# Kernel optimization log

Measured on AMD Instinct MI355X. Metric: run time of the kernel, lower is better.

## Reference

```python
import jax, jax.numpy as jnp
import numpy as np

START_TAG = 2
STOP_TAG = 3
NEG = -10000.0


def _lstm_dir(x, w_ih, w_hh, b_ih, b_hh, h0, c0):
    """Single-direction LSTM over x:[T,F]. PyTorch gate order i,f,g,o."""
    xp = x @ w_ih.T + b_ih  # [T, 4H] - big GEMM done once

    def step(carry, xt):
        h, c = carry
        g = xt + h @ w_hh.T + b_hh
        i, f, gg, o = jnp.split(g, 4)
        c = jax.nn.sigmoid(f) * c + jax.nn.sigmoid(i) * jnp.tanh(gg)
        h = jax.nn.sigmoid(o) * jnp.tanh(c)
        return (h, c), h

    _, hs = jax.lax.scan(step, (h0, c0), xp)
    return hs  # [T, H]


def _viterbi(feats, transitions):
    # feats: [T, n_tags]; transitions[next, prev]
    n = transitions.shape[0]
    init = jnp.full((n,), NEG, feats.dtype).at[START_TAG].set(0.0)

    def step(fv, feat):
        scores = fv[None, :] + transitions          # [next, prev]
        bptr = jnp.argmax(scores, axis=1)           # best prev per next
        return jnp.max(scores, axis=1) + feat, bptr

    fv, bptrs = jax.lax.scan(step, init, feats)
    terminal = fv + transitions[STOP_TAG]
    best = jnp.argmax(terminal)
    score = terminal[best]

    def back(tag, bp):
        return bp[tag], tag  # emit tag at step t, carry tag at t-1

    _, path = jax.lax.scan(back, best, bptrs, reverse=True)
    return score, path  # scalar, [T] int32


def setup_inputs() -> dict:
    key = jax.random.key(0)
    T, F, H = 4096, 1024, 2048
    H2 = H // 2
    NTAG = 4
    ks = jax.random.split(key, 16)
    s_ih = 1.0 / np.sqrt(H2)

    def u(k, shape, s):
        return jax.random.uniform(k, shape, jnp.float32, -s, s)

    transitions = jax.random.normal(ks[13], (NTAG, NTAG), jnp.float32)
    transitions = transitions.at[START_TAG, :].set(NEG)
    transitions = transitions.at[:, STOP_TAG].set(NEG)

    return {
        "sentence": jax.random.normal(ks[0], (T, F), jnp.float32),
        "h0": jax.random.normal(ks[1], (2, 1, H2), jnp.float32),
        "c0": jax.random.normal(ks[2], (2, 1, H2), jnp.float32),
        "w_ih_f": u(ks[3], (4 * H2, F), s_ih),
        "w_hh_f": u(ks[4], (4 * H2, H2), s_ih),
        "b_ih_f": u(ks[5], (4 * H2,), s_ih),
        "b_hh_f": u(ks[6], (4 * H2,), s_ih),
        "w_ih_b": u(ks[7], (4 * H2, F), s_ih),
        "w_hh_b": u(ks[8], (4 * H2, H2), s_ih),
        "b_ih_b": u(ks[9], (4 * H2,), s_ih),
        "b_hh_b": u(ks[10], (4 * H2,), s_ih),
        "w_tag": u(ks[11], (NTAG, H), 1.0 / np.sqrt(H)),
        "b_tag": u(ks[12], (NTAG,), 1.0 / np.sqrt(H)),
        "transitions": transitions,
    }


def reference(sentence, h0, c0, w_ih_f, w_hh_f, b_ih_f, b_hh_f,
              w_ih_b, w_hh_b, b_ih_b, b_hh_b, w_tag, b_tag, transitions):
    # Bidirectional LSTM, batch=1 (torch stacks directions on dim 0 of h0/c0)
    h_fwd = _lstm_dir(sentence, w_ih_f, w_hh_f, b_ih_f, b_hh_f, h0[0, 0], c0[0, 0])
    h_bwd = _lstm_dir(sentence[::-1], w_ih_b, w_hh_b, b_ih_b, b_hh_b, h0[1, 0], c0[1, 0])[::-1]
    lstm_out = jnp.concatenate([h_fwd, h_bwd], axis=-1)  # [T, hidden_dim]
    feats = lstm_out @ w_tag.T + b_tag                    # [T, 4]
    score, path = _viterbi(feats, transitions)
    return score, path
```

## Files before the change

### kernel.cpp

```cpp
#include <hip/hip_runtime.h>
#include <cstddef>
#include <cstdint>

#define T_LEN 4096
#define FDIM  1024
#define H2DIM 1024
#define GDIM  4096

#define NEGV (-10000.0f)
#define START_TAG 2
#define STOP_TAG 3

#define XP_OFF      ((size_t)0)
#define XP_BYTES    ((size_t)2 * T_LEN * GDIM * 4)
#define HIST_OFF    (XP_OFF + XP_BYTES)
#define HIST_BYTES  ((size_t)T_LEN * 2048 * 4)
#define FEATS_OFF   (HIST_OFF + HIST_BYTES)
#define FEATS_BYTES ((size_t)T_LEN * 4 * 4)
#define SLOTS_OFF   (FEATS_OFF + FEATS_BYTES)
#define SLOTS_BYTES ((size_t)2 * 2 * 1024 * 8)
#define WS_NEED     (SLOTS_OFF + SLOTS_BYTES)

__device__ __forceinline__ float sigm(float x) { return 1.0f / (1.0f + expf(-x)); }

__global__ __launch_bounds__(256)
void xp_gemm(const float* __restrict__ x,
             const float* __restrict__ w_f, const float* __restrict__ w_b,
             const float* __restrict__ bi_f, const float* __restrict__ bh_f,
             const float* __restrict__ bi_b, const float* __restrict__ bh_b,
             float* __restrict__ xp)
{
    const int tid = threadIdx.x;
    const int dir = blockIdx.z;
    const int j0  = blockIdx.x * 128;
    const int t0  = blockIdx.y * 128;
    const float* __restrict__ w  = dir ? w_b  : w_f;
    const float* __restrict__ bi = dir ? bi_b : bi_f;
    const float* __restrict__ bh = dir ? bh_b : bh_f;

    __shared__ float As[32][133];
    __shared__ float Bs[32][133];

    const int tm0 = (tid & 15) * 8;
    const int tn0 = (tid >> 4) * 8;

    float acc[8][8];
    #pragma unroll
    for (int i = 0; i < 8; ++i)
        #pragma unroll
        for (int j = 0; j < 8; ++j) acc[i][j] = 0.f;

    const int lrow = tid >> 3;
    const int lkq  = (tid & 7) * 4;

    for (int kb = 0; kb < FDIM; kb += 32) {
        #pragma unroll
        for (int hh = 0; hh < 4; ++hh) {
            const int r  = lrow + hh * 32;
            const int tg = t0 + r;
            const int sr = dir ? (T_LEN - 1 - tg) : tg;
            const float4 av = *(const float4*)&x[(size_t)sr * FDIM + kb + lkq];
            As[lkq+0][r] = av.x; As[lkq+1][r] = av.y; As[lkq+2][r] = av.z; As[lkq+3][r] = av.w;
            const float4 bv = *(const float4*)&w[(size_t)(j0 + r) * FDIM + kb + lkq];
            Bs[lkq+0][r] = bv.x; Bs[lkq+1][r] = bv.y; Bs[lkq+2][r] = bv.z; Bs[lkq+3][r] = bv.w;
        }
        __syncthreads();
        #pragma unroll
        for (int k = 0; k < 32; ++k) {
            const float4 a0 = *(const float4*)&As[k][tm0];
            const float4 a1 = *(const float4*)&As[k][tm0 + 4];
            const float4 b0 = *(const float4*)&Bs[k][tn0];
            const float4 b1 = *(const float4*)&Bs[k][tn0 + 4];
            const float av[8] = {a0.x,a0.y,a0.z,a0.w,a1.x,a1.y,a1.z,a1.w};
            const float bv[8] = {b0.x,b0.y,b0.z,b0.w,b1.x,b1.y,b1.z,b1.w};
            #pragma unroll
            for (int i = 0; i < 8; ++i)
                #pragma unroll
                for (int j = 0; j < 8; ++j) acc[i][j] += av[i] * bv[j];
        }
        __syncthreads();
    }

    float bias[8];
    #pragma unroll
    for (int j = 0; j < 8; ++j) { const int col = j0 + tn0 + j; bias[j] = bi[col] + bh[col]; }

    float* __restrict__ xpd = xp + (size_t)dir * T_LEN * GDIM;
    #pragma unroll
    for (int i = 0; i < 8; ++i) {
        const int tr = t0 + tm0 + i;
        float4 o0, o1;
        o0.x = acc[i][0] + bias[0]; o0.y = acc[i][1] + bias[1];
        o0.z = acc[i][2] + bias[2]; o0.w = acc[i][3] + bias[3];
        o1.x = acc[i][4] + bias[4]; o1.y = acc[i][5] + bias[5];
        o1.z = acc[i][6] + bias[6]; o1.w = acc[i][7] + bias[7];
        *(float4*)&xpd[(size_t)tr * GDIM + j0 + tn0]     = o0;
        *(float4*)&xpd[(size_t)tr * GDIM + j0 + tn0 + 4] = o1;
    }
}

__global__ __launch_bounds__(256, 1)
void lstm_scan(const float* __restrict__ xp,
               const float* __restrict__ h0,
               const float* __restrict__ c0,
               const float* __restrict__ whh_f,
               const float* __restrict__ whh_b,
               float* __restrict__ hist,
               unsigned long long* __restrict__ slots)
{
    __shared__ float wsl[32][1024];
    __shared__ float hbuf[1024];
    __shared__ float gsh[32];

    const int tid = threadIdx.x;
    const int b   = blockIdx.x;
    const int dir = b >> 7;
    const int bi  = b & 127;
    const int u0  = bi * 8;
    const int rg  = tid >> 5;
    const int kc  = tid & 31;
    const int lrb = rg * 4;

    const float* __restrict__ whh = dir ? whh_b : whh_f;
    const size_t xpbase = (size_t)dir * T_LEN * GDIM;

    for (int lr = 0; lr < 32; ++lr) {
        const int grow = ((lr >> 3) << 10) + u0 + (lr & 7);
        *(float4*)&wsl[lr][tid * 4] = *(const float4*)&whh[(size_t)grow * H2DIM + tid * 4];
    }
    *(float4*)&hbuf[tid * 4] = *(const float4*)&h0[dir * H2DIM + tid * 4];
    float creg = 0.f;
    if (tid < 8) creg = c0[dir * H2DIM + u0 + tid];

    int grows[4];
    #pragma unroll
    for (int j = 0; j < 4; ++j) {
        const int lr = lrb + j;
        grows[j] = ((lr >> 3) << 10) + u0 + (lr & 7);
    }
    float xpc[4] = {0.f, 0.f, 0.f, 0.f};
    if (kc == 0) {
        #pragma unroll
        for (int j = 0; j < 4; ++j) xpc[j] = xp[xpbase + grows[j]];
    }
    __syncthreads();

    int budget = 4000000;

    for (int t = 0; t < T_LEN; ++t) {
        float xpn[4] = {0.f, 0.f, 0.f, 0.f};
        const int tnx = (t + 1 < T_LEN) ? (t + 1) : t;
        if (kc == 0) {
            #pragma unroll
            for (int j = 0; j < 4; ++j) xpn[j] = xp[xpbase + (size_t)tnx * GDIM + grows[j]];
        }

        float p0 = 0.f, p1 = 0.f, p2 = 0.f, p3 = 0.f;
        #pragma unroll
        for (int s = 0; s < 8; ++s) {
            const int ko = s * 128 + kc * 4;
            const float4 hv = *(const float4*)&hbuf[ko];
            const float4 w0 = *(const float4*)&wsl[lrb + 0][ko];
            const float4 w1 = *(const float4*)&wsl[lrb + 1][ko];
            const float4 w2 = *(const float4*)&wsl[lrb + 2][ko];
            const float4 w3 = *(const float4*)&wsl[lrb + 3][ko];
            p0 += w0.x*hv.x + w0.y*hv.y + w0.z*hv.z + w0.w*hv.w;
            p1 += w1.x*hv.x + w1.y*hv.y + w1.z*hv.z + w1.w*hv.w;
            p2 += w2.x*hv.x + w2.y*hv.y + w2.z*hv.z + w2.w*hv.w;
            p3 += w3.x*hv.x + w3.y*hv.y + w3.z*hv.z + w3.w*hv.w;
        }
        #pragma unroll
        for (int m = 16; m >= 1; m >>= 1) {
            p0 += __shfl_xor(p0, m);
            p1 += __shfl_xor(p1, m);
            p2 += __shfl_xor(p2, m);
            p3 += __shfl_xor(p3, m);
        }
        if (kc == 0) {
            gsh[lrb + 0] = p0 + xpc[0];
            gsh[lrb + 1] = p1 + xpc[1];
            gsh[lrb + 2] = p2 + xpc[2];
            gsh[lrb + 3] = p3 + xpc[3];
        }
        __syncthreads();

        if (tid < 8) {
            const float gi = gsh[tid];
            const float gf = gsh[8 + tid];
            const float gg = gsh[16 + tid];
            const float go = gsh[24 + tid];
            const float c  = sigm(gf) * creg + sigm(gi) * tanhf(gg);
            const float h  = sigm(go) * tanhf(c);
            creg = c;
            const int tg = dir ? (T_LEN - 1 - t) : t;
            hist[(size_t)tg * 2048 + dir * H2DIM + u0 + tid] = h;
            const unsigned long long pack =
                ((unsigned long long)(unsigned)(t + 1) << 32) |
                (unsigned long long)__float_as_uint(h);
            __hip_atomic_store(&slots[((size_t)((t + 1) & 1) * 2 + dir) * H2DIM + u0 + tid],
                               pack, __ATOMIC_RELAXED, __HIP_MEMORY_SCOPE_AGENT);
        }

        if (t + 1 < T_LEN) {
            const unsigned want = (unsigned)(t + 1);
            unsigned long long* sb = &slots[((size_t)((t + 1) & 1) * 2 + dir) * H2DIM + tid * 4];
            unsigned long long v0 = 0, v1 = 0, v2 = 0, v3 = 0;
            bool g0 = false, g1 = false, g2 = false, g3 = false;
            for (;;) {
                if (!g0) v0 = __hip_atomic_load(&sb[0], __ATOMIC_RELAXED, __HIP_MEMORY_SCOPE_AGENT);
                if (!g1) v1 = __hip_atomic_load(&sb[1], __ATOMIC_RELAXED, __HIP_MEMORY_SCOPE_AGENT);
                if (!g2) v2 = __hip_atomic_load(&sb[2], __ATOMIC_RELAXED, __HIP_MEMORY_SCOPE_AGENT);
                if (!g3) v3 = __hip_atomic_load(&sb[3], __ATOMIC_RELAXED, __HIP_MEMORY_SCOPE_AGENT);
                g0 = g0 || ((unsigned)(v0 >> 32) == want);
                g1 = g1 || ((unsigned)(v1 >> 32) == want);
                g2 = g2 || ((unsigned)(v2 >> 32) == want);
                g3 = g3 || ((unsigned)(v3 >> 32) == want);
                if (g0 && g1 && g2 && g3) break;
                if (--budget <= 0) break;
                __builtin_amdgcn_s_sleep(1);
            }
            float4 hv;
            hv.x = __uint_as_float((unsigned)v0);
            hv.y = __uint_as_float((unsigned)v1);
            hv.z = __uint_as_float((unsigned)v2);
            hv.w = __uint_as_float((unsigned)v3);
            *(float4*)&hbuf[tid * 4] = hv;
        }
        __syncthreads();
        if (kc == 0) { xpc[0] = xpn[0]; xpc[1] = xpn[1]; xpc[2] = xpn[2]; xpc[3] = xpn[3]; }
    }
}

__global__ __launch_bounds__(256)
void feats_kernel(const float* __restrict__ hist,
                  const float* __restrict__ w_tag,
                  const float* __restrict__ b_tag,
                  float* __restrict__ feats)
{
    const int t = blockIdx.x;
    const int tid = threadIdx.x;
    const float* __restrict__ hrow = hist + (size_t)t * 2048 + tid * 8;
    const float4 ha = *(const float4*)&hrow[0];
    const float4 hb = *(const float4*)&hrow[4];
    float p[4];
    #pragma unroll
    for (int n = 0; n < 4; ++n) {
        const float* __restrict__ wr = w_tag + n * 2048 + tid * 8;
        const float4 wa = *(const float4*)&wr[0];
        const float4 wb = *(const float4*)&wr[4];
        p[n] = ha.x*wa.x + ha.y*wa.y + ha.z*wa.z + ha.w*wa.w
             + hb.x*wb.x + hb.y*wb.y + hb.z*wb.z + hb.w*wb.w;
    }
    #pragma unroll
    for (int m = 32; m >= 1; m >>= 1) {
        #pragma unroll
        for (int n = 0; n < 4; ++n) p[n] += __shfl_down(p[n], m);
    }
    __shared__ float red[4][4];
    const int wv = tid >> 6;
    if ((tid & 63) == 0) {
        #pragma unroll
        for (int n = 0; n < 4; ++n) red[n][wv] = p[n];
    }
    __syncthreads();
    if (tid < 4)
        feats[(size_t)t * 4 + tid] = red[tid][0] + red[tid][1] + red[tid][2] + red[tid][3] + b_tag[tid];
}

__global__ __launch_bounds__(256)
void viterbi_kernel(const float* __restrict__ feats,
                    const float* __restrict__ trans,
                    float* __restrict__ out)
{
    __shared__ float fsh[T_LEN * 4];
    __shared__ unsigned bp[T_LEN];
    const int tid = threadIdx.x;
    for (int i = tid; i < T_LEN; i += 256)
        *(float4*)&fsh[i * 4] = *(const float4*)&feats[(size_t)i * 4];
    __syncthreads();
    if (tid == 0) {
        float tr[16];
        #pragma unroll
        for (int i = 0; i < 16; ++i) tr[i] = trans[i];
        float fv[4] = {NEGV, NEGV, NEGV, NEGV};
        fv[START_TAG] = 0.0f;
        for (int t = 0; t < T_LEN; ++t) {
            float nf[4]; unsigned pb = 0;
            #pragma unroll
            for (int n = 0; n < 4; ++n) {
                float m = fv[0] + tr[n * 4 + 0]; int bsel = 0;
                #pragma unroll
                for (int p = 1; p < 4; ++p) {
                    const float s = fv[p] + tr[n * 4 + p];
                    if (s > m) { m = s; bsel = p; }
                }
                nf[n] = m + fsh[t * 4 + n];
                pb |= (unsigned)bsel << (8 * n);
            }
            bp[t] = pb;
            fv[0] = nf[0]; fv[1] = nf[1]; fv[2] = nf[2]; fv[3] = nf[3];
        }
        float bm = fv[0] + tr[STOP_TAG * 4 + 0]; int best = 0;
        #pragma unroll
        for (int p = 1; p < 4; ++p) {
            const float s = fv[p] + tr[STOP_TAG * 4 + p];
            if (s > bm) { bm = s; best = p; }
        }
        out[0] = bm;
        int cur = best;
        for (int t = T_LEN - 1; t >= 0; --t) {
            out[1 + t] = (float)cur;
            cur = (int)((bp[t] >> (8 * cur)) & 0xffu);
        }
    }
}

extern "C" void kernel_launch(void* const* d_in, const int* in_sizes, int n_in,
                              void* d_out, int out_size, void* d_ws, size_t ws_size,
                              hipStream_t stream) {
    const float* x      = (const float*)d_in[0];
    const float* h0     = (const float*)d_in[1];
    const float* c0     = (const float*)d_in[2];
    const float* w_ih_f = (const float*)d_in[3];
    const float* w_hh_f = (const float*)d_in[4];
    const float* b_ih_f = (const float*)d_in[5];
    const float* b_hh_f = (const float*)d_in[6];
    const float* w_ih_b = (const float*)d_in[7];
    const float* w_hh_b = (const float*)d_in[8];
    const float* b_ih_b = (const float*)d_in[9];
    const float* b_hh_b = (const float*)d_in[10];
    const float* w_tag  = (const float*)d_in[11];
    const float* b_tag  = (const float*)d_in[12];
    const float* trans  = (const float*)d_in[13];
    float* out = (float*)d_out;

    if (ws_size < WS_NEED) return;

    char* ws = (char*)d_ws;
    float* xp    = (float*)(ws + XP_OFF);
    float* hist  = (float*)(ws + HIST_OFF);
    float* feats = (float*)(ws + FEATS_OFF);
    unsigned long long* slots = (unsigned long long*)(ws + SLOTS_OFF);

    hipMemsetAsync(slots, 0, SLOTS_BYTES, stream);

    dim3 ggrid(32, 32, 2);
    xp_gemm<<<ggrid, 256, 0, stream>>>(x, w_ih_f, w_ih_b, b_ih_f, b_hh_f, b_ih_b, b_hh_b, xp);

    void* ka[] = { (void*)&xp, (void*)&h0, (void*)&c0, (void*)&w_hh_f, (void*)&w_hh_b,
                   (void*)&hist, (void*)&slots };
    hipLaunchCooperativeKernel((void*)lstm_scan, dim3(256), dim3(256), ka, 0, stream);

    feats_kernel<<<T_LEN, 256, 0, stream>>>(hist, w_tag, b_tag, feats);
    viterbi_kernel<<<1, 256, 0, stream>>>(feats, trans, out);
}
```

Before: 15.29 ms.

## Hold recurrent weights in registers and drop mid-step barrier via per-unit warps

The recurrent LSTM scan now keeps each 32-lane group's four gate rows of W_hh in registers instead of LDS, and each group owns one hidden unit. A transpose-style shuffle reduction leaves all four gate sums in lane 0, which computes the cell update directly. This removes the shared gate buffer and one __syncthreads per step. hbuf is double-buffered so the remaining barrier suffices. The cost is heavy register use (128 floats of weights per thread), with a risk of spills at 256 threads.

```diff
diff --git a/kernel.cpp b/kernel.cpp
--- a/kernel.cpp
+++ b/kernel.cpp
@@ -108,9 +108,7 @@
                float* __restrict__ hist,
                unsigned long long* __restrict__ slots)
 {
-    __shared__ float wsl[32][1024];
-    __shared__ float hbuf[1024];
-    __shared__ float gsh[32];
+    __shared__ float hbuf[2][1024];
 
     const int tid = threadIdx.x;
     const int b   = blockIdx.x;
@@ -119,103 +117,103 @@
     const int u0  = bi * 8;
     const int rg  = tid >> 5;
     const int kc  = tid & 31;
-    const int lrb = rg * 4;
 
     const float* __restrict__ whh = dir ? whh_b : whh_f;
     const size_t xpbase = (size_t)dir * T_LEN * GDIM;
-
-    for (int lr = 0; lr < 32; ++lr) {
-        const int grow = ((lr >> 3) << 10) + u0 + (lr & 7);
-        *(float4*)&wsl[lr][tid * 4] = *(const float4*)&whh[(size_t)grow * H2DIM + tid * 4];
-    }
-    *(float4*)&hbuf[tid * 4] = *(const float4*)&h0[dir * H2DIM + tid * 4];
+    const int unit = u0 + rg;
+
+    float4 wr[4][8];
+    #pragma unroll
+    for (int g = 0; g < 4; ++g) {
+        const float* __restrict__ row = whh + ((size_t)(g << 10) + unit) * H2DIM;
+        #pragma unroll
+        for (int s = 0; s < 8; ++s)
+            wr[g][s] = *(const float4*)&row[s * 128 + kc * 4];
+    }
+
+    *(float4*)&hbuf[0][tid * 4] = *(const float4*)&h0[dir * H2DIM + tid * 4];
     float creg = 0.f;
-    if (tid < 8) creg = c0[dir * H2DIM + u0 + tid];
-
-    int grows[4];
-    #pragma unroll
-    for (int j = 0; j < 4; ++j) {
-        const int lr = lrb + j;
-        grows[j] = ((lr >> 3) << 10) + u0 + (lr & 7);
-    }
     float xpc[4] = {0.f, 0.f, 0.f, 0.f};
     if (kc == 0) {
-        #pragma unroll
-        for (int j = 0; j < 4; ++j) xpc[j] = xp[xpbase + grows[j]];
+        creg = c0[dir * H2DIM + unit];
+        #pragma unroll
+        for (int g = 0; g < 4; ++g) xpc[g] = xp[xpbase + (g << 10) + unit];
     }
     __syncthreads();
 
     int budget = 4000000;
 
     for (int t = 0; t < T_LEN; ++t) {
+        const float* __restrict__ hb = hbuf[t & 1];
+
         float xpn[4] = {0.f, 0.f, 0.f, 0.f};
         const int tnx = (t + 1 < T_LEN) ? (t + 1) : t;
         if (kc == 0) {
             #pragma unroll
-            for (int j = 0; j < 4; ++j) xpn[j] = xp[xpbase + (size_t)tnx * GDIM + grows[j]];
+            for (int g = 0; g < 4; ++g)
+                xpn[g] = xp[xpbase + (size_t)tnx * GDIM + (g << 10) + unit];
         }
 
         float p0 = 0.f, p1 = 0.f, p2 = 0.f, p3 = 0.f;
         #pragma unroll
         for (int s = 0; s < 8; ++s) {
-            const int ko = s * 128 + kc * 4;
-            const float4 hv = *(const float4*)&hbuf[ko];
-            const float4 w0 = *(const float4*)&wsl[lrb + 0][ko];
-            const float4 w1 = *(const float4*)&wsl[lrb + 1][ko];
-            const float4 w2 = *(const float4*)&wsl[lrb + 2][ko];
-            const float4 w3 = *(const float4*)&wsl[lrb + 3][ko];
-            p0 += w0.x*hv.x + w0.y*hv.y + w0.z*hv.z + w0.w*hv.w;
-            p1 += w1.x*hv.x + w1.y*hv.y + w1.z*hv.z + w1.w*hv.w;
-            p2 += w2.x*hv.x + w2.y*hv.y + w2.z*hv.z + w2.w*hv.w;
-            p3 += w3.x*hv.x + w3.y*hv.y + w3.z*hv.z + w3.w*hv.w;
-        }
-        #pragma unroll
-        for (int m = 16; m >= 1; m >>= 1) {
-            p0 += __shfl_xor(p0, m);
-            p1 += __shfl_xor(p1, m);
-            p2 += __shfl_xor(p2, m);
-            p3 += __shfl_xor(p3, m);
-        }
+            const float4 hv = *(const float4*)&hb[s * 128 + kc * 4];
+            p0 += wr[0][s].x*hv.x + wr[0][s].y*hv.y + wr[0][s].z*hv.z + wr[0][s].w*hv.w;
+            p1 += wr[1][s].x*hv.x + wr[1][s].y*hv.y + wr[1][s].z*hv.z + wr[1][s].w*hv.w;
+            p2 += wr[2][s].x*hv.x + wr[2][s].y*hv.y + wr[2][s].z*hv.z + wr[2][s].w*hv.w;
+            p3 += wr[3][s].x*hv.x + wr[3][s].y*hv.y + wr[3][s].z*hv.z + wr[3][s].w*hv.w;
+        }
+
+        const bool o1 = (kc & 1);
+        float sa = o1 ? p0 : p1;
+        float ra = __shfl_xor(sa, 1);
+        float qa = (o1 ? p1 : p0) + ra;
+        float sb = o1 ? p2 : p3;
+        float rb = __shfl_xor(sb, 1);
+        float qb = (o1 ? p3 : p2) + rb;
+        const bool o2 = (kc & 2);
+        float sc = o2 ? qa : qb;
+        float rc = __shfl_xor(sc, 2);
+        float r  = (o2 ? qb : qa) + rc;
+        r += __shfl_xor(r, 4);
+        r += __shfl_xor(r, 8);
+        r += __shfl_xor(r, 16);
+        const float g1 = __shfl_xor(r, 1);
+        const float g2 = __shfl_xor(r, 2);
+        const float g3 = __shfl_xor(r, 3);
+
         if (kc == 0) {
-            gsh[lrb + 0] = p0 + xpc[0];
-            gsh[lrb + 1] = p1 + xpc[1];
-            gsh[lrb + 2] = p2 + xpc[2];
-            gsh[lrb + 3] = p3 + xpc[3];
-        }
-        __syncthreads();
-
-        if (tid < 8) {
-            const float gi = gsh[tid];
-            const float gf = gsh[8 + tid];
-            const float gg = gsh[16 + tid];
-            const float go = gsh[24 + tid];
+            const float gi = r  + xpc[0];
+            const float gf = g1 + xpc[1];
+            const float gg = g2 + xpc[2];
+            const float go = g3 + xpc[3];
             const float c  = sigm(gf) * creg + sigm(gi) * tanhf(gg);
             const float h  = sigm(go) * tanhf(c);
             creg = c;
             const int tg = dir ? (T_LEN - 1 - t) : t;
-            hist[(size_t)tg * 2048 + dir * H2DIM + u0 + tid] = h;
+            hist[(size_t)tg * 2048 + dir * H2DIM + unit] = h;
             const unsigned long long pack =
                 ((unsigned long long)(unsigned)(t + 1) << 32) |
                 (unsigned long long)__float_as_uint(h);
-            __hip_atomic_store(&slots[((size_t)((t + 1) & 1) * 2 + dir) * H2DIM + u0 + tid],
+            __hip_atomic_store(&slots[((size_t)((t + 1) & 1) * 2 + dir) * H2DIM + unit],
                                pack, __ATOMIC_RELAXED, __HIP_MEMORY_SCOPE_AGENT);
         }
 
         if (t + 1 < T_LEN) {
             const unsigned want = (unsigned)(t + 1);
-            unsigned long long* sb = &slots[((size_t)((t + 1) & 1) * 2 + dir) * H2DIM + tid * 4];
+            unsigned long long* sb4 = &slots[((size_t)((t + 1) & 1) * 2 + dir) * H2DIM + tid * 4];
             unsigned long long v0 = 0, v1 = 0, v2 = 0, v3 = 0;
-            bool g0 = false, g1 = false, g2 = false, g3 = false;
+            bool d0 = false, d1 = false, d2 = false, d3 = false;
             for (;;) {
-                if (!g0) v0 = __hip_atomic_load(&sb[0], __ATOMIC_RELAXED, __HIP_MEMORY_SCOPE_AGENT);
-                if (!g1) v1 = __hip_atomic_load(&sb[1], __ATOMIC_RELAXED, __HIP_MEMORY_SCOPE_AGENT);
-                if (!g2) v2 = __hip_atomic_load(&sb[2], __ATOMIC_RELAXED, __HIP_MEMORY_SCOPE_AGENT);
-                if (!g3) v3 = __hip_atomic_load(&sb[3], __ATOMIC_RELAXED, __HIP_MEMORY_SCOPE_AGENT);
-                g0 = g0 || ((unsigned)(v0 >> 32) == want);
-                g1 = g1 || ((unsigned)(v1 >> 32) == want);
-                g2 = g2 || ((unsigned)(v2 >> 32) == want);
-                g3 = g3 || ((unsigned)(v3 >> 32) == want);
-                if (g0 && g1 && g2 && g3) break;
+                if (!d0) v0 = __hip_atomic_load(&sb4[0], __ATOMIC_RELAXED, __HIP_MEMORY_SCOPE_AGENT);
+                if (!d1) v1 = __hip_atomic_load(&sb4[1], __ATOMIC_RELAXED, __HIP_MEMORY_SCOPE_AGENT);
+                if (!d2) v2 = __hip_atomic_load(&sb4[2], __ATOMIC_RELAXED, __HIP_MEMORY_SCOPE_AGENT);
+                if (!d3) v3 = __hip_atomic_load(&sb4[3], __ATOMIC_RELAXED, __HIP_MEMORY_SCOPE_AGENT);
+                d0 = d0 || ((unsigned)(v0 >> 32) == want);
+                d1 = d1 || ((unsigned)(v1 >> 32) == want);
+                d2 = d2 || ((unsigned)(v2 >> 32) == want);
+                d3 = d3 || ((unsigned)(v3 >> 32) == want);
+                if (d0 && d1 && d2 && d3) break;
                 if (--budget <= 0) break;
                 __builtin_amdgcn_s_sleep(1);
             }
@@ -224,10 +222,11 @@
             hv.y = __uint_as_float((unsigned)v1);
             hv.z = __uint_as_float((unsigned)v2);
             hv.w = __uint_as_float((unsigned)v3);
-            *(float4*)&hbuf[tid * 4] = hv;
+            *(float4*)&hbuf[(t + 1) & 1][tid * 4] = hv;
         }
         __syncthreads();
-        if (kc == 0) { xpc[0] = xpn[0]; xpc[1] = xpn[1]; xpc[2] = xpn[2]; xpc[3] = xpn[3]; }
+        #pragma unroll
+        for (int g = 0; g < 4; ++g) xpc[g] = xpn[g];
     }
 }
 
```

After: 19.42 ms. 1.27x slower.

## Replace FP32 input-projection GEMM with bf16 MFMA kernel plus conversion passes

Applied to the files above, without the earlier changes.

Converts the sentence and both input weight matrices to bf16 in scratch space (reusing the hist region before the scan runs). The input-projection GEMM then runs on MFMA 16x16x32 bf16 instructions, one wavefront per 64x64 tile, with operands loaded straight from global memory and no LDS. The aim is to cut the cost of the large FP32 SIMT GEMM. In exchange it adds three conversion kernels and bf16 rounding error, which then feeds the long recurrent scan and the Viterbi argmax.

```diff
diff --git a/kernel.cpp b/kernel.cpp
--- a/kernel.cpp
+++ b/kernel.cpp
@@ -21,81 +21,97 @@
 #define SLOTS_BYTES ((size_t)2 * 2 * 1024 * 8)
 #define WS_NEED     (SLOTS_OFF + SLOTS_BYTES)
 
+#define XB_OFF      (HIST_OFF)
+#define WBF_OFF     (HIST_OFF + (size_t)8  * 1024 * 1024)
+#define WBB_OFF     (HIST_OFF + (size_t)16 * 1024 * 1024)
+
 __device__ __forceinline__ float sigm(float x) { return 1.0f / (1.0f + expf(-x)); }
 
+__device__ __forceinline__ unsigned short f2bf(float f) {
+    unsigned u = __float_as_uint(f);
+    return (unsigned short)((u + 0x7FFFu + ((u >> 16) & 1u)) >> 16);
+}
+
+typedef short  bf16x8 __attribute__((ext_vector_type(8)));
+typedef float  f32x4  __attribute__((ext_vector_type(4)));
+
 __global__ __launch_bounds__(256)
-void xp_gemm(const float* __restrict__ x,
-             const float* __restrict__ w_f, const float* __restrict__ w_b,
-             const float* __restrict__ bi_f, const float* __restrict__ bh_f,
-             const float* __restrict__ bi_b, const float* __restrict__ bh_b,
-             float* __restrict__ xp)
-{
-    const int tid = threadIdx.x;
-    const int dir = blockIdx.z;
-    const int j0  = blockIdx.x * 128;
-    const int t0  = blockIdx.y * 128;
-    const float* __restrict__ w  = dir ? w_b  : w_f;
+void conv_bf16(const float* __restrict__ src, unsigned short* __restrict__ dst, int n4)
+{
+    int i = blockIdx.x * 256 + threadIdx.x;
+    const int stride = gridDim.x * 256;
+    for (; i < n4; i += stride) {
+        const float4 v = ((const float4*)src)[i];
+        ushort4 o;
+        o.x = f2bf(v.x); o.y = f2bf(v.y); o.z = f2bf(v.z); o.w = f2bf(v.w);
+        ((ushort4*)dst)[i] = o;
+    }
+}
+
+__global__ __launch_bounds__(64)
+void xp_gemm_mfma(const unsigned short* __restrict__ xb,
+                  const unsigned short* __restrict__ wb_f,
+                  const unsigned short* __restrict__ wb_b,
+                  const float* __restrict__ bi_f, const float* __restrict__ bh_f,
+                  const float* __restrict__ bi_b, const float* __restrict__ bh_b,
+                  float* __restrict__ xp)
+{
+    const int lane = threadIdx.x;
+    const int j0   = blockIdx.x * 64;
+    const int t0   = blockIdx.y * 64;
+    const int dir  = blockIdx.z;
+    const unsigned short* __restrict__ wb = dir ? wb_b : wb_f;
     const float* __restrict__ bi = dir ? bi_b : bi_f;
     const float* __restrict__ bh = dir ? bh_b : bh_f;
 
-    __shared__ float As[32][133];
-    __shared__ float Bs[32][133];
-
-    const int tm0 = (tid & 15) * 8;
-    const int tn0 = (tid >> 4) * 8;
-
-    float acc[8][8];
-    #pragma unroll
-    for (int i = 0; i < 8; ++i)
-        #pragma unroll
-        for (int j = 0; j < 8; ++j) acc[i][j] = 0.f;
-
-    const int lrow = tid >> 3;
-    const int lkq  = (tid & 7) * 4;
-
-    for (int kb = 0; kb < FDIM; kb += 32) {
-        #pragma unroll
-        for (int hh = 0; hh < 4; ++hh) {
-            const int r  = lrow + hh * 32;
-            const int tg = t0 + r;
-            const int sr = dir ? (T_LEN - 1 - tg) : tg;
-            const float4 av = *(const float4*)&x[(size_t)sr * FDIM + kb + lkq];
-            As[lkq+0][r] = av.x; As[lkq+1][r] = av.y; As[lkq+2][r] = av.z; As[lkq+3][r] = av.w;
-            const float4 bv = *(const float4*)&w[(size_t)(j0 + r) * FDIM + kb + lkq];
-            Bs[lkq+0][r] = bv.x; Bs[lkq+1][r] = bv.y; Bs[lkq+2][r] = bv.z; Bs[lkq+3][r] = bv.w;
-        }
-        __syncthreads();
-        #pragma unroll
-        for (int k = 0; k < 32; ++k) {
-            const float4 a0 = *(const float4*)&As[k][tm0];
-            const float4 a1 = *(const float4*)&As[k][tm0 + 4];
-            const float4 b0 = *(const float4*)&Bs[k][tn0];
-            const float4 b1 = *(const float4*)&Bs[k][tn0 + 4];
-            const float av[8] = {a0.x,a0.y,a0.z,a0.w,a1.x,a1.y,a1.z,a1.w};
-            const float bv[8] = {b0.x,b0.y,b0.z,b0.w,b1.x,b1.y,b1.z,b1.w};
+    const int r  = lane & 15;
+    const int kg = lane >> 4;
+
+    const unsigned short* arow[4];
+    const unsigned short* brow[4];
+    #pragma unroll
+    for (int s = 0; s < 4; ++s) {
+        const int tg = t0 + s * 16 + r;
+        const int sr = dir ? (T_LEN - 1 - tg) : tg;
+        arow[s] = xb + (size_t)sr * FDIM + kg * 8;
+        brow[s] = wb + (size_t)(j0 + s * 16 + r) * FDIM + kg * 8;
+    }
+
+    f32x4 acc[4][4];
+    #pragma unroll
+    for (int sm = 0; sm < 4; ++sm)
+        #pragma unroll
+        for (int sn = 0; sn < 4; ++sn)
+            acc[sm][sn] = (f32x4){0.f, 0.f, 0.f, 0.f};
+
+    for (int k0 = 0; k0 < FDIM; k0 += 32) {
+        bf16x8 a[4], b[4];
+        #pragma unroll
+        for (int s = 0; s < 4; ++s) {
+            a[s] = *(const bf16x8*)(arow[s] + k0);
+            b[s] = *(const bf16x8*)(brow[s] + k0);
+        }
+        #pragma unroll
+        for (int sm = 0; sm < 4; ++sm)
             #pragma unroll
-            for (int i = 0; i < 8; ++i)
-                #pragma unroll
-                for (int j = 0; j < 8; ++j) acc[i][j] += av[i] * bv[j];
-        }
-        __syncthreads();
-    }
-
-    float bias[8];
-    #pragma unroll
-    for (int j = 0; j < 8; ++j) { const int col = j0 + tn0 + j; bias[j] = bi[col] + bh[col]; }
+            for (int sn = 0; sn < 4; ++sn)
+                acc[sm][sn] = __builtin_amdgcn_mfma_f32_16x16x32_bf16(
+                                  a[sm], b[sn], acc[sm][sn], 0, 0, 0);
+    }
 
     float* __restrict__ xpd = xp + (size_t)dir * T_LEN * GDIM;
     #pragma unroll
-    for (int i = 0; i < 8; ++i) {
-        const int tr = t0 + tm0 + i;
-        float4 o0, o1;
-        o0.x = acc[i][0] + bias[0]; o0.y = acc[i][1] + bias[1];
-        o0.z = acc[i][2] + bias[2]; o0.w = acc[i][3] + bias[3];
-        o1.x = acc[i][4] + bias[4]; o1.y = acc[i][5] + bias[5];
-        o1.z = acc[i][6] + bias[6]; o1.w = acc[i][7] + bias[7];
-        *(float4*)&xpd[(size_t)tr * GDIM + j0 + tn0]     = o0;
-        *(float4*)&xpd[(size_t)tr * GDIM + j0 + tn0 + 4] = o1;
+    for (int sn = 0; sn < 4; ++sn) {
+        const int col  = j0 + sn * 16 + r;
+        const float bv = bi[col] + bh[col];
+        #pragma unroll
+        for (int sm = 0; sm < 4; ++sm) {
+            #pragma unroll
+            for (int j = 0; j < 4; ++j) {
+                const int row = t0 + sm * 16 + kg * 4 + j;
+                xpd[(size_t)row * GDIM + col] = acc[sm][sn][j] + bv;
+            }
+        }
     }
 }
 
@@ -341,11 +357,19 @@
     float* hist  = (float*)(ws + HIST_OFF);
     float* feats = (float*)(ws + FEATS_OFF);
     unsigned long long* slots = (unsigned long long*)(ws + SLOTS_OFF);
+    unsigned short* xb  = (unsigned short*)(ws + XB_OFF);
+    unsigned short* wbf = (unsigned short*)(ws + WBF_OFF);
+    unsigned short* wbb = (unsigned short*)(ws + WBB_OFF);
 
     hipMemsetAsync(slots, 0, SLOTS_BYTES, stream);
 
-    dim3 ggrid(32, 32, 2);
-    xp_gemm<<<ggrid, 256, 0, stream>>>(x, w_ih_f, w_ih_b, b_ih_f, b_hh_f, b_ih_b, b_hh_b, xp);
+    const int n4 = (T_LEN * FDIM) / 4;
+    conv_bf16<<<1024, 256, 0, stream>>>(x,      xb,  n4);
+    conv_bf16<<<1024, 256, 0, stream>>>(w_ih_f, wbf, n4);
+    conv_bf16<<<1024, 256, 0, stream>>>(w_ih_b, wbb, n4);
+
+    xp_gemm_mfma<<<dim3(64, 64, 2), 64, 0, stream>>>(
+        xb, wbf, wbb, b_ih_f, b_hh_f, b_ih_b, b_hh_b, xp);
 
     void* ka[] = { (void*)&xp, (void*)&h0, (void*)&c0, (void*)&w_hh_f, (void*)&w_hh_b,
                    (void*)&hist, (void*)&slots };
```

Result: faster. 14.33 ms (-6.3%).
